# Optimization experiments

Measured on AMD Instinct MI355X. Metric: run time of the kernel, lower is better.

The kernel has to match this reference:

```python
import jax, jax.numpy as jnp
import numpy as np

D_MODEL = 1024
NUM_HEADS = 16
D_K = D_MODEL // NUM_HEADS
THETA = 10000.0


def _rope(x, pos):
    # x: [B, H, T, d_k], pos: [T]
    inv_freq = 1.0 / (THETA ** (jnp.arange(0, D_K, 2, dtype=jnp.float32) / D_K))  # [d_k/2]
    ang = pos.astype(jnp.float32)[:, None] * inv_freq[None, :]                    # [T, d_k/2]
    cos = jnp.repeat(jnp.cos(ang), 2, axis=-1)                                    # [T, d_k]
    sin = jnp.repeat(jnp.sin(ang), 2, axis=-1)
    x = x.astype(jnp.float32)
    x0 = x[..., ::2]
    x1 = x[..., 1::2]
    rot = jnp.stack((-x1, x0), axis=-1).reshape(x.shape)  # rotate_half, interleaved
    return x * cos + rot * sin


def setup_inputs() -> dict:
    key = jax.random.key(0)
    k1, k2, k3 = jax.random.split(key, 3)
    B, T = 2, 2048
    sigma_qkv = float(np.sqrt(2.0 / (D_MODEL + 3 * D_MODEL)))
    sigma_out = float(np.sqrt(2.0 / (D_MODEL + D_MODEL)))
    return {
        "x": jax.random.normal(k1, (B, T, D_MODEL), dtype=jnp.float32),
        "w_qkv": jax.random.normal(k2, (3 * D_MODEL, D_MODEL), dtype=jnp.float32) * sigma_qkv,
        "w_out": jax.random.normal(k3, (D_MODEL, D_MODEL), dtype=jnp.float32) * sigma_out,
    }


def reference(x, w_qkv, w_out):
    B, T, _ = x.shape
    qkv = jnp.einsum("btd,ed->bte", x, w_qkv)                 # [B, T, 3*D]
    q, k, v = jnp.split(qkv, 3, axis=-1)

    def split_head(t):
        return t.reshape(B, T, NUM_HEADS, D_K).transpose(0, 2, 1, 3)  # [B, H, T, d_k]

    q, k, v = split_head(q), split_head(k), split_head(v)
    pos = jnp.arange(T)
    q = _rope(q, pos)
    k = _rope(k, pos)

    scores = jnp.einsum("bhqd,bhkd->bhqk", q, k) / jnp.sqrt(jnp.float32(D_K))
    causal = jnp.tril(jnp.ones((T, T), dtype=bool))            # True = keep
    scores = jnp.where(causal[None, None], scores, -jnp.inf)
    attn = jax.nn.softmax(scores, axis=-1)
    out = jnp.einsum("bhqk,bhkd->bhqd", attn, v)               # [B, H, T, d_k]
    out = out.transpose(0, 2, 1, 3).reshape(B, T, D_MODEL)
    return jnp.einsum("btd,ed->bte", out, w_out)
```

## Files before the change

kernel.cpp:

```cpp
#include <hip/hip_runtime.h>
#include <cstdint>
#include <cstddef>

#define BB 2
#define TT 2048
#define DMODEL 1024
#define NHEADS 16
#define DK 64

typedef short short8 __attribute__((ext_vector_type(8)));
typedef unsigned short ushort8 __attribute__((ext_vector_type(8)));
typedef float floatx4 __attribute__((ext_vector_type(4)));
typedef _Float16 half4 __attribute__((ext_vector_type(4)));
typedef float float2v __attribute__((ext_vector_type(2)));

#define MFMA_PV(A, B, C) __builtin_amdgcn_mfma_f32_16x16x16f16(A, B, C, 0, 0, 0)

__device__ __forceinline__ unsigned short f2bf(float f) {
    uint32_t u = __builtin_bit_cast(uint32_t, f);
    uint32_t r = (u + 0x7FFFu + ((u >> 16) & 1u)) >> 16;
    return (unsigned short)r;
}
__device__ __forceinline__ float bf2f(unsigned short s) {
    uint32_t u = ((uint32_t)s) << 16;
    return __builtin_bit_cast(float, u);
}

#define GLDS16(g, l) __builtin_amdgcn_global_load_lds( \
    (const __attribute__((address_space(1))) void*)(g), \
    (__attribute__((address_space(3))) void*)(l), 16, 0, 0)

__global__ void castk3(const float* __restrict__ x, unsigned short* __restrict__ xb,
                       const float* __restrict__ wq, unsigned short* __restrict__ wqb,
                       const float* __restrict__ wo, unsigned short* __restrict__ wob) {
    int bid = blockIdx.x;
    const float* in;
    unsigned short* out;
    int base;
    if (bid < 4096)       { in = x;  out = xb;  base = bid * 1024; }
    else if (bid < 7168)  { in = wq; out = wqb; base = (bid - 4096) * 1024; }
    else                  { in = wo; out = wob; base = (bid - 7168) * 1024; }
    int i = base + threadIdx.x * 4;
    float4 v = *(const float4*)(in + i);
    ushort4 o;
    o.x = f2bf(v.x); o.y = f2bf(v.y); o.z = f2bf(v.z); o.w = f2bf(v.w);
    *(ushort4*)(out + i) = o;
}

template <typename OUT>
__global__ __launch_bounds__(256)
void gemm_bt(const unsigned short* __restrict__ A, const unsigned short* __restrict__ B,
             OUT* __restrict__ C, int M, int N, int K) {
    __shared__ unsigned short As[128 * 32];
    __shared__ unsigned short Bs[128 * 32];

    const int tid  = threadIdx.x;
    const int lane = tid & 63;
    const int w    = tid >> 6;
    const int wm   = w & 1;
    const int wn   = w >> 1;
    const int quad = lane >> 4;
    const int l16  = lane & 15;

    const int m0 = blockIdx.y * 128;
    const int n0 = blockIdx.x * 128;

    floatx4 acc[4][4];
#pragma unroll
    for (int a = 0; a < 4; a++)
#pragma unroll
        for (int b = 0; b < 4; b++)
            acc[a][b] = (floatx4){0.f, 0.f, 0.f, 0.f};

    const int c0 = w * 128 + lane;
    const int c1 = c0 + 64;
    const int r0 = c0 >> 2, cc0 = (c0 & 3) ^ ((r0 >> 1) & 3);
    const int r1 = c1 >> 2, cc1 = (c1 & 3) ^ ((r1 >> 1) & 3);

    const unsigned short* gA0 = A + (size_t)(m0 + r0) * K + cc0 * 8;
    const unsigned short* gA1 = A + (size_t)(m0 + r1) * K + cc1 * 8;
    const unsigned short* gB0 = B + (size_t)(n0 + r0) * K + cc0 * 8;
    const unsigned short* gB1 = B + (size_t)(n0 + r1) * K + cc1 * 8;

    unsigned short* lA0 = &As[(2 * w + 0) * 512];
    unsigned short* lA1 = &As[(2 * w + 1) * 512];
    unsigned short* lB0 = &Bs[(2 * w + 0) * 512];
    unsigned short* lB1 = &Bs[(2 * w + 1) * 512];

    const int rsw = (l16 >> 1) & 3;

    for (int k0 = 0; k0 < K; k0 += 32) {
        __syncthreads();
        GLDS16(gA0 + k0, lA0);
        GLDS16(gA1 + k0, lA1);
        GLDS16(gB0 + k0, lB0);
        GLDS16(gB1 + k0, lB1);
        __syncthreads();

        short8 af[4], bf[4];
#pragma unroll
        for (int t = 0; t < 4; t++) {
            af[t] = *(const short8*)&As[(wm * 64 + t * 16 + l16) * 32 + (quad ^ rsw) * 8];
            bf[t] = *(const short8*)&Bs[(wn * 64 + t * 16 + l16) * 32 + (quad ^ rsw) * 8];
        }
#pragma unroll
        for (int tm = 0; tm < 4; tm++)
#pragma unroll
            for (int tn = 0; tn < 4; tn++)
                acc[tm][tn] = __builtin_amdgcn_mfma_f32_16x16x32_bf16(
                    af[tm], bf[tn], acc[tm][tn], 0, 0, 0);
    }

#pragma unroll
    for (int tm = 0; tm < 4; tm++) {
#pragma unroll
        for (int tn = 0; tn < 4; tn++) {
#pragma unroll
            for (int r = 0; r < 4; r++) {
                int m = m0 + wm * 64 + tm * 16 + quad * 4 + r;
                int n = n0 + wn * 64 + tn * 16 + l16;
                if constexpr (sizeof(OUT) == 4)
                    C[(size_t)m * N + n] = acc[tm][tn][r];
                else
                    C[(size_t)m * N + n] = f2bf(acc[tm][tn][r]);
            }
        }
    }
}

__global__ __launch_bounds__(512)
void gemm256(const unsigned short* __restrict__ A, const unsigned short* __restrict__ B,
             unsigned short* __restrict__ C, int M, int N, int K) {
    __shared__ unsigned short As[2][2][8192];
    __shared__ unsigned short Bs[2][2][8192];

    const int tid  = threadIdx.x;
    const int lane = tid & 63;
    const int w    = tid >> 6;
    const int wm   = w >> 2;
    const int wn   = w & 3;
    const int quad = lane >> 4;
    const int l16  = lane & 15;

    const int gx  = gridDim.x;
    const int bid = blockIdx.y * gx + blockIdx.x;
    const int cpx = (gx * gridDim.y) >> 3;
    const int wg  = (bid & 7) * cpx + (bid >> 3);
    const int m0  = (wg / gx) * 256;
    const int n0  = (wg % gx) * 256;

    floatx4 acc[8][4];
#pragma unroll
    for (int a = 0; a < 8; a++)
#pragma unroll
        for (int b = 0; b < 4; b++)
            acc[a][b] = (floatx4){0.f, 0.f, 0.f, 0.f};

    const int r1   = tid >> 3;
    const int koff = ((tid & 7) ^ (r1 & 7)) * 8;
    const unsigned short* Ag = A + (size_t)(m0 + r1) * K + koff;
    const unsigned short* Bg = B + (size_t)(n0 + r1) * K + koff;
    const int NT2 = K >> 6;

#define STAGE_A(dd, hh, kt) { \
    GLDS16(Ag + (size_t)((hh) * 128) * K + (kt) * 64,      &As[dd][hh][tid * 8]); \
    GLDS16(Ag + (size_t)((hh) * 128 + 64) * K + (kt) * 64, &As[dd][hh][4096 + tid * 8]); }
#define STAGE_B(dd, hh, kt) { \
    GLDS16(Bg + (size_t)((hh) * 128) * K + (kt) * 64,      &Bs[dd][hh][tid * 8]); \
    GLDS16(Bg + (size_t)((hh) * 128 + 64) * K + (kt) * 64, &Bs[dd][hh][4096 + tid * 8]); }

#define BARRIER() __builtin_amdgcn_s_barrier()

    STAGE_B(0, 0, 0); STAGE_B(0, 1, 0);
    STAGE_A(0, 0, 0); STAGE_A(0, 1, 0);
    STAGE_B(1, 0, 1); STAGE_B(1, 1, 1);
    asm volatile("s_waitcnt vmcnt(4)" ::: "memory");
    BARRIER();

    const int c0    = (quad ^ (l16 & 7)) * 8;
    const int bhalf = wn >> 1;
    const int brow0 = (wn & 1) * 64 + l16;

    short8 a[8], b[8];

    for (int it = 0; it < NT2; ++it) {
        const int d = it & 1;

#pragma unroll
        for (int nfl = 0; nfl < 2; nfl++)
#pragma unroll
            for (int ks = 0; ks < 2; ks++)
                b[2 * nfl + ks] = *(const short8*)&Bs[d][bhalf][(brow0 + nfl * 16) * 64 + (c0 ^ (ks * 32))];
#pragma unroll
        for (int mfl = 0; mfl < 4; mfl++)
#pragma unroll
            for (int ks = 0; ks < 2; ks++)
                a[2 * mfl + ks] = *(const short8*)&As[d][wm][(l16 + mfl * 16) * 64 + (c0 ^ (ks * 32))];
        if (it + 1 < NT2) STAGE_A(d ^ 1, 0, it + 1);
        BARRIER();
        __builtin_amdgcn_s_setprio(1);
#pragma unroll
        for (int mfl = 0; mfl < 4; mfl++)
#pragma unroll
            for (int nf = 0; nf < 2; nf++) {
                acc[mfl][nf] = __builtin_amdgcn_mfma_f32_16x16x32_bf16(a[2 * mfl], b[2 * nf], acc[mfl][nf], 0, 0, 0);
                acc[mfl][nf] = __builtin_amdgcn_mfma_f32_16x16x32_bf16(a[2 * mfl + 1], b[2 * nf + 1], acc[mfl][nf], 0, 0, 0);
            }
        __builtin_amdgcn_s_setprio(0);
        BARRIER();

#pragma unroll
        for (int nfl = 0; nfl < 2; nfl++)
#pragma unroll
            for (int ks = 0; ks < 2; ks++)
                b[4 + 2 * nfl + ks] = *(const short8*)&Bs[d][bhalf][(brow0 + 32 + nfl * 16) * 64 + (c0 ^ (ks * 32))];
        if (it + 1 < NT2) STAGE_A(d ^ 1, 1, it + 1);
        BARRIER();
        __builtin_amdgcn_s_setprio(1);
#pragma unroll
        for (int mfl = 0; mfl < 4; mfl++)
#pragma unroll
            for (int nf = 2; nf < 4; nf++) {
                acc[mfl][nf] = __builtin_amdgcn_mfma_f32_16x16x32_bf16(a[2 * mfl], b[2 * nf], acc[mfl][nf], 0, 0, 0);
                acc[mfl][nf] = __builtin_amdgcn_mfma_f32_16x16x32_bf16(a[2 * mfl + 1], b[2 * nf + 1], acc[mfl][nf], 0, 0, 0);
            }
        __builtin_amdgcn_s_setprio(0);
        BARRIER();

#pragma unroll
        for (int mfl = 0; mfl < 4; mfl++)
#pragma unroll
            for (int ks = 0; ks < 2; ks++)
                a[2 * mfl + ks] = *(const short8*)&As[d][wm][(64 + l16 + mfl * 16) * 64 + (c0 ^ (ks * 32))];
        if (it + 2 < NT2) STAGE_B(d, 0, it + 2);
        BARRIER();
        __builtin_amdgcn_s_setprio(1);
#pragma unroll
        for (int mfl = 0; mfl < 4; mfl++)
#pragma unroll
            for (int nf = 0; nf < 2; nf++) {
                acc[4 + mfl][nf] = __builtin_amdgcn_mfma_f32_16x16x32_bf16(a[2 * mfl], b[2 * nf], acc[4 + mfl][nf], 0, 0, 0);
                acc[4 + mfl][nf] = __builtin_amdgcn_mfma_f32_16x16x32_bf16(a[2 * mfl + 1], b[2 * nf + 1], acc[4 + mfl][nf], 0, 0, 0);
            }
        __builtin_amdgcn_s_setprio(0);
        BARRIER();

        if (it + 2 < NT2) STAGE_B(d, 1, it + 2);
        if (it < NT2 - 2) {
            asm volatile("s_waitcnt vmcnt(4)" ::: "memory");
        } else if (it == NT2 - 2) {
            asm volatile("s_waitcnt vmcnt(0)" ::: "memory");
        }
        BARRIER();
        __builtin_amdgcn_s_setprio(1);
#pragma unroll
        for (int mfl = 0; mfl < 4; mfl++)
#pragma unroll
            for (int nf = 2; nf < 4; nf++) {
                acc[4 + mfl][nf] = __builtin_amdgcn_mfma_f32_16x16x32_bf16(a[2 * mfl], b[2 * nf], acc[4 + mfl][nf], 0, 0, 0);
                acc[4 + mfl][nf] = __builtin_amdgcn_mfma_f32_16x16x32_bf16(a[2 * mfl + 1], b[2 * nf + 1], acc[4 + mfl][nf], 0, 0, 0);
            }
        __builtin_amdgcn_s_setprio(0);
        BARRIER();
    }
#undef STAGE_A
#undef STAGE_B
#undef BARRIER

#pragma unroll
    for (int mf = 0; mf < 8; mf++) {
#pragma unroll
        for (int nf = 0; nf < 4; nf++) {
#pragma unroll
            for (int r = 0; r < 4; r++) {
                int m = m0 + wm * 128 + mf * 16 + quad * 4 + r;
                int n = n0 + wn * 64 + nf * 16 + l16;
                C[(size_t)m * N + n] = f2bf(acc[mf][nf][r]);
            }
        }
    }
}

__global__ __launch_bounds__(256)
void ropevt(const unsigned short* __restrict__ qkv,
            unsigned short* __restrict__ qb, unsigned short* __restrict__ kb,
            unsigned short* __restrict__ vtb) {
    __shared__ unsigned short tile[64][72];
    const int tid = threadIdx.x;
    const int bh  = blockIdx.y;
    const int b = bh >> 4, h = bh & 15;
    const int t0 = blockIdx.x * 64;

    const float QS = 0.18033688f;
#pragma unroll
    for (int rep = 0; rep < 8; rep++) {
        int idx  = rep * 256 + tid;
        int p    = idx & 31;
        int trow = idx >> 5;
        int t    = t0 + trow;

        size_t src = (size_t)(b * TT + t) * 3072 + h * 64 + 2 * p;
        ushort2 qu = *(const ushort2*)(qkv + src);
        ushort2 ku = *(const ushort2*)(qkv + src + 1024);
        float qx = bf2f(qu.x), qy = bf2f(qu.y);
        float kx = bf2f(ku.x), ky = bf2f(ku.y);

        float invf = __powf(10000.f, -((float)(2 * p)) / 64.f);
        float ang  = (float)t * invf;
        float sn, cs;
        __sincosf(ang, &sn, &cs);

        size_t dst = ((size_t)bh * TT + t) * 64 + 2 * p;
        ushort2 qo, ko;
        qo.x = f2bf((qx * cs - qy * sn) * QS); qo.y = f2bf((qy * cs + qx * sn) * QS);
        ko.x = f2bf(kx * cs - ky * sn); ko.y = f2bf(ky * cs + kx * sn);
        *(ushort2*)(qb + dst) = qo;
        *(ushort2*)(kb + dst) = ko;
    }

    const int row = tid >> 2;
    const unsigned short* src = qkv + ((size_t)(b * TT) + t0 + row) * 3072 + 2048 + h * 64;
    {
        int cb = (tid & 3) * 16;
        ushort8 v0 = *(const ushort8*)(src + cb);
        ushort8 v1 = *(const ushort8*)(src + cb + 8);
#pragma unroll
        for (int i = 0; i < 8; i++) tile[row][cb + i] = v0[i];
#pragma unroll
        for (int i = 0; i < 8; i++) tile[row][cb + 8 + i] = v1[i];
    }
    __syncthreads();

    const int d  = tid >> 2;
    const int tc = tid & 3;
    const int hs = (d & 1) * 4;
    ushort8 o0, o1;
#pragma unroll
    for (int i = 0; i < 8; i++) {
        _Float16 hv = (_Float16)bf2f(tile[tc * 16 + (i ^ hs)][d]);
        o0[i] = __builtin_bit_cast(unsigned short, hv);
    }
#pragma unroll
    for (int i = 0; i < 8; i++) {
        _Float16 hv = (_Float16)bf2f(tile[tc * 16 + 8 + (i ^ hs)][d]);
        o1[i] = __builtin_bit_cast(unsigned short, hv);
    }
    unsigned short* dst = vtb + ((size_t)bh * 64 + d) * TT + t0 + tc * 16;
    *(ushort8*)(dst) = o0;
    *(ushort8*)(dst + 8) = o1;
}

__global__ __launch_bounds__(256, 3)
void attn_mfma(const unsigned short* __restrict__ qb,
               const unsigned short* __restrict__ kb,
               const unsigned short* __restrict__ vtb,
               unsigned short* __restrict__ out) {
    __shared__ unsigned short Ks[3][64 * 64];
    __shared__ unsigned short Vs[3][64 * 64];

    const int tid  = threadIdx.x;
    const int lane = tid & 63;
    const int w    = tid >> 6;
    const int quad = lane >> 4;
    const int l16  = lane & 15;

    const int bh    = blockIdx.x;
    const int qtile = gridDim.y - 1 - blockIdx.y;
    const int q0    = qtile * 64;

    const unsigned short* Qp = qb + ((size_t)bh * TT + q0 + w * 16) * 64;
    const unsigned short* Kp = kb + (size_t)bh * TT * 64;
    const unsigned short* Vp = vtb + (size_t)bh * 64 * TT;

    short8 aq[2];
#pragma unroll
    for (int ks = 0; ks < 2; ks++)
        aq[ks] = *(const short8*)(Qp + (size_t)l16 * 64 + ks * 32 + quad * 8);

    floatx4 Oacc[4];
#pragma unroll
    for (int dt = 0; dt < 4; dt++) Oacc[dt] = (floatx4){0.f, 0.f, 0.f, 0.f};
    floatx4 lacc = (floatx4){0.f, 0.f, 0.f, 0.f};

    const int ntiles = qtile + 1;

    const int cs0 = tid, cs1 = 256 + tid;
    const int rK0 = cs0 >> 3, sK0 = cs0 & 7;
    const int rK1 = cs1 >> 3, sK1 = cs1 & 7;
    const unsigned short* gk0 = Kp + rK0 * 64 + (sK0 ^ (rK0 & 7)) * 8;
    const unsigned short* gk1 = Kp + rK1 * 64 + (sK1 ^ (rK1 & 7)) * 8;
    const unsigned short* gv0 = Vp + (size_t)rK0 * TT + (sK0 ^ ((rK0 >> 1) & 7)) * 8;
    const unsigned short* gv1 = Vp + (size_t)rK1 * TT + (sK1 ^ ((rK1 >> 1) & 7)) * 8;
    const int ld0 = cs0 * 8, ld1 = cs1 * 8;

#define STAGE(IT, P)                                      \
    {                                                     \
        GLDS16(gk0 + (size_t)(IT) * 4096, &Ks[P][ld0]);   \
        GLDS16(gv0 + (IT) * 64,           &Vs[P][ld0]);   \
        GLDS16(gk1 + (size_t)(IT) * 4096, &Ks[P][ld1]);   \
        GLDS16(gv1 + (IT) * 64,           &Vs[P][ld1]);   \
    }

    STAGE(0, 0);
    if (ntiles > 1) {
        STAGE(1, 1);
        asm volatile("s_waitcnt vmcnt(4)" ::: "memory");
    } else {
        asm volatile("s_waitcnt vmcnt(0)" ::: "memory");
    }
    __builtin_amdgcn_s_barrier();

    const int ksw  = l16 & 7;
    const int vsw  = (l16 >> 1) & 7;
    const int vsub = ((quad & 1) ^ (l16 & 1)) * 4;
    const int kofs0 = (l16 * 64 + ((quad) ^ ksw) * 8) * 2;
    const int kofs1 = (l16 * 64 + ((4 + quad) ^ ksw) * 8) * 2;
    const int qh    = quad >> 1;
    const int vofs0 = (l16 * 64 + ((0 + qh) ^ vsw) * 8 + vsub) * 2;
    const int vofs1 = (l16 * 64 + ((2 + qh) ^ vsw) * 8 + vsub) * 2;
    const int vofs2 = (l16 * 64 + ((4 + qh) ^ vsw) * 8 + vsub) * 2;
    const int vofs3 = (l16 * 64 + ((6 + qh) ^ vsw) * 8 + vsub) * 2;

    const half4 vones = (half4){(_Float16)1.f, (_Float16)1.f, (_Float16)1.f, (_Float16)1.f};

    int p = 0, p2 = 2;

    for (int it = 0; it < ntiles; ++it) {
        if (it + 2 < ntiles) STAGE(it + 2, p2);

        const char* Kb = (const char*)Ks + p * 8192;
        const char* Vb = (const char*)Vs + p * 8192;

        floatx4 sacc[4];
#pragma unroll
        for (int nt = 0; nt < 4; nt++) sacc[nt] = (floatx4){0.f, 0.f, 0.f, 0.f};

#pragma unroll
        for (int ks = 0; ks < 2; ks++)
#pragma unroll
            for (int nt = 0; nt < 4; nt++) {
                short8 kf = *(const short8*)(Kb + (ks ? kofs1 : kofs0) + nt * 2048);
                sacc[nt] = __builtin_amdgcn_mfma_f32_16x16x32_bf16(kf, aq[ks], sacc[nt], 0, 0, 0);
            }

        if (it == qtile) {
            const int qg = w * 16 + l16;
#pragma unroll
            for (int nt = 0; nt < 4; nt++)
#pragma unroll
                for (int r = 0; r < 4; r++)
                    if (nt * 16 + quad * 4 + r > qg) sacc[nt][r] = -1e30f;
        }

#pragma unroll
        for (int nt = 0; nt < 4; nt++)
#pragma unroll
            for (int r = 0; r < 4; r++)
                sacc[nt][r] = __builtin_amdgcn_exp2f(sacc[nt][r]);

        half4 bp[4];
#pragma unroll
        for (int nt = 0; nt < 4; nt++) {
            float lo = __builtin_bit_cast(float, __builtin_amdgcn_cvt_pkrtz(sacc[nt][0], sacc[nt][1]));
            float hi = __builtin_bit_cast(float, __builtin_amdgcn_cvt_pkrtz(sacc[nt][2], sacc[nt][3]));
            float2v f2;
            f2[0] = lo;
            f2[1] = hi;
            bp[nt] = __builtin_bit_cast(half4, f2);
        }

        {
            floatx4 lsum;
#pragma unroll
            for (int r = 0; r < 4; r++)
                lsum[r] = (sacc[0][r] + sacc[1][r]) + (sacc[2][r] + sacc[3][r]);
            float llo = __builtin_bit_cast(float, __builtin_amdgcn_cvt_pkrtz(lsum[0], lsum[1]));
            float lhi = __builtin_bit_cast(float, __builtin_amdgcn_cvt_pkrtz(lsum[2], lsum[3]));
            float2v lf2;
            lf2[0] = llo;
            lf2[1] = lhi;
            half4 pl = __builtin_bit_cast(half4, lf2);
            lacc = MFMA_PV(vones, pl, lacc);
        }

#pragma unroll
        for (int dt = 0; dt < 4; dt++)
#pragma unroll
            for (int nt = 0; nt < 4; nt++) {
                const int vo = (nt == 0) ? vofs0 : (nt == 1) ? vofs1 : (nt == 2) ? vofs2 : vofs3;
                half4 vf = *(const half4*)(Vb + vo + dt * 2048);
                Oacc[dt] = MFMA_PV(vf, bp[nt], Oacc[dt]);
            }

        if (it + 1 < ntiles) {
            if (it + 2 < ntiles) {
                asm volatile("s_waitcnt vmcnt(4)" ::: "memory");
            } else {
                asm volatile("s_waitcnt vmcnt(0)" ::: "memory");
            }
            __builtin_amdgcn_s_barrier();
        }
        p  = (p == 2) ? 0 : p + 1;
        p2 = (p2 == 2) ? 0 : p2 + 1;
    }
#undef STAGE

    const int b = bh >> 4, h = bh & 15;
    const float inv = 1.f / lacc[0];
    const size_t base = ((size_t)(b * TT + q0 + w * 16 + l16)) * DMODEL + h * 64 + quad * 4;
#pragma unroll
    for (int dt = 0; dt < 4; dt++) {
        ushort4 pk;
        pk.x = f2bf(Oacc[dt][0] * inv);
        pk.y = f2bf(Oacc[dt][1] * inv);
        pk.z = f2bf(Oacc[dt][2] * inv);
        pk.w = f2bf(Oacc[dt][3] * inv);
        *(ushort4*)(out + base + dt * 16) = pk;
    }
}

extern "C" void kernel_launch(void* const* d_in, const int* in_sizes, int n_in,
                              void* d_out, int out_size, void* d_ws, size_t ws_size,
                              hipStream_t stream) {
    const float* x     = (const float*)d_in[0];
    const float* w_qkv = (const float*)d_in[1];
    const float* w_out = (const float*)d_in[2];
    float* out = (float*)d_out;

    char* ws = (char*)d_ws;

    unsigned short* xb   = (unsigned short*)(ws);
    unsigned short* wqb  = (unsigned short*)(ws + 8388608);
    unsigned short* wob  = (unsigned short*)(ws + 14680064);
    unsigned short* qkvb = (unsigned short*)(ws + 16777216);
    unsigned short* qb   = (unsigned short*)(ws + 41943040);
    unsigned short* kb   = (unsigned short*)(ws + 50331648);
    unsigned short* vtb  = (unsigned short*)(ws + 58720256);
    unsigned short* attb = (unsigned short*)(ws + 67108864);

    castk3<<<8192, 256, 0, stream>>>(x, xb, w_qkv, wqb, w_out, wob);

    gemm256<<<dim3(3072 / 256, 4096 / 256), 512, 0, stream>>>(
        xb, wqb, qkvb, 4096, 3072, 1024);

    ropevt<<<dim3(TT / 64, BB * NHEADS), 256, 0, stream>>>(qkvb, qb, kb, vtb);

    attn_mfma<<<dim3(BB * NHEADS, TT / 64), 256, 0, stream>>>(qb, kb, vtb, attb);

    gemm_bt<float><<<dim3(1024 / 128, 4096 / 128), 256, 0, stream>>>(
        attb, wob, out, 4096, 1024, 1024);
}
```

Measured before the change: 181.1 us.

## Read K and V fragments directly from global memory, dropping LDS staging

The attention kernel stops staging K and V tiles into a triple-buffered shared-memory ring with async global-to-LDS loads and barriers. Each wave now loads its MFMA operand fragments straight from global memory and relies on the cache for reuse across the four waves. The occupancy hint goes up from 3 to 4 blocks per CU because no LDS is used. The cost is redundant global loads per wave and no software prefetch, so load latency is exposed inside the loop.

```diff
diff --git a/kernel.cpp b/kernel.cpp
--- a/kernel.cpp
+++ b/kernel.cpp
@@ -350,14 +350,11 @@
     *(ushort8*)(dst + 8) = o1;
 }
 
-__global__ __launch_bounds__(256, 3)
+__global__ __launch_bounds__(256, 4)
 void attn_mfma(const unsigned short* __restrict__ qb,
                const unsigned short* __restrict__ kb,
                const unsigned short* __restrict__ vtb,
                unsigned short* __restrict__ out) {
-    __shared__ unsigned short Ks[3][64 * 64];
-    __shared__ unsigned short Vs[3][64 * 64];
-
     const int tid  = threadIdx.x;
     const int lane = tid & 63;
     const int w    = tid >> 6;
@@ -384,52 +381,15 @@
 
     const int ntiles = qtile + 1;
 
-    const int cs0 = tid, cs1 = 256 + tid;
-    const int rK0 = cs0 >> 3, sK0 = cs0 & 7;
-    const int rK1 = cs1 >> 3, sK1 = cs1 & 7;
-    const unsigned short* gk0 = Kp + rK0 * 64 + (sK0 ^ (rK0 & 7)) * 8;
-    const unsigned short* gk1 = Kp + rK1 * 64 + (sK1 ^ (rK1 & 7)) * 8;
-    const unsigned short* gv0 = Vp + (size_t)rK0 * TT + (sK0 ^ ((rK0 >> 1) & 7)) * 8;
-    const unsigned short* gv1 = Vp + (size_t)rK1 * TT + (sK1 ^ ((rK1 >> 1) & 7)) * 8;
-    const int ld0 = cs0 * 8, ld1 = cs1 * 8;
-
-#define STAGE(IT, P)                                      \
-    {                                                     \
-        GLDS16(gk0 + (size_t)(IT) * 4096, &Ks[P][ld0]);   \
-        GLDS16(gv0 + (IT) * 64,           &Vs[P][ld0]);   \
-        GLDS16(gk1 + (size_t)(IT) * 4096, &Ks[P][ld1]);   \
-        GLDS16(gv1 + (IT) * 64,           &Vs[P][ld1]);   \
-    }
-
-    STAGE(0, 0);
-    if (ntiles > 1) {
-        STAGE(1, 1);
-        asm volatile("s_waitcnt vmcnt(4)" ::: "memory");
-    } else {
-        asm volatile("s_waitcnt vmcnt(0)" ::: "memory");
-    }
-    __builtin_amdgcn_s_barrier();
-
-    const int ksw  = l16 & 7;
-    const int vsw  = (l16 >> 1) & 7;
     const int vsub = ((quad & 1) ^ (l16 & 1)) * 4;
-    const int kofs0 = (l16 * 64 + ((quad) ^ ksw) * 8) * 2;
-    const int kofs1 = (l16 * 64 + ((4 + quad) ^ ksw) * 8) * 2;
-    const int qh    = quad >> 1;
-    const int vofs0 = (l16 * 64 + ((0 + qh) ^ vsw) * 8 + vsub) * 2;
-    const int vofs1 = (l16 * 64 + ((2 + qh) ^ vsw) * 8 + vsub) * 2;
-    const int vofs2 = (l16 * 64 + ((4 + qh) ^ vsw) * 8 + vsub) * 2;
-    const int vofs3 = (l16 * 64 + ((6 + qh) ^ vsw) * 8 + vsub) * 2;
+    const unsigned short* kbase = Kp + (size_t)l16 * 64 + quad * 8;
+    const unsigned short* vbase = Vp + (size_t)l16 * TT + (quad >> 1) * 8 + vsub;
 
     const half4 vones = (half4){(_Float16)1.f, (_Float16)1.f, (_Float16)1.f, (_Float16)1.f};
 
-    int p = 0, p2 = 2;
-
     for (int it = 0; it < ntiles; ++it) {
-        if (it + 2 < ntiles) STAGE(it + 2, p2);
-
-        const char* Kb = (const char*)Ks + p * 8192;
-        const char* Vb = (const char*)Vs + p * 8192;
+        const unsigned short* kt = kbase + (size_t)it * 4096;
+        const unsigned short* vt = vbase + it * 64;
 
         floatx4 sacc[4];
 #pragma unroll
@@ -439,7 +399,7 @@
         for (int ks = 0; ks < 2; ks++)
 #pragma unroll
             for (int nt = 0; nt < 4; nt++) {
-                short8 kf = *(const short8*)(Kb + (ks ? kofs1 : kofs0) + nt * 2048);
+                short8 kf = *(const short8*)(kt + nt * 1024 + ks * 32);
                 sacc[nt] = __builtin_amdgcn_mfma_f32_16x16x32_bf16(kf, aq[ks], sacc[nt], 0, 0, 0);
             }
 
@@ -487,23 +447,10 @@
         for (int dt = 0; dt < 4; dt++)
 #pragma unroll
             for (int nt = 0; nt < 4; nt++) {
-                const int vo = (nt == 0) ? vofs0 : (nt == 1) ? vofs1 : (nt == 2) ? vofs2 : vofs3;
-                half4 vf = *(const half4*)(Vb + vo + dt * 2048);
+                half4 vf = *(const half4*)(vt + (size_t)dt * 16 * TT + nt * 16);
                 Oacc[dt] = MFMA_PV(vf, bp[nt], Oacc[dt]);
             }
-
-        if (it + 1 < ntiles) {
-            if (it + 2 < ntiles) {
-                asm volatile("s_waitcnt vmcnt(4)" ::: "memory");
-            } else {
-                asm volatile("s_waitcnt vmcnt(0)" ::: "memory");
-            }
-            __builtin_amdgcn_s_barrier();
-        }
-        p  = (p == 2) ? 0 : p + 1;
-        p2 = (p2 == 2) ? 0 : p2 + 1;
-    }
-#undef STAGE
+    }
 
     const int b = bh >> 4, h = bh & 15;
     const float inv = 1.f / lacc[0];
```

Result: slower. 293.2 us (+61.9%).
